# Performance work log

Hardware: AMD Instinct MI355X
Metric: run time of the kernel (lower is better)

Reference implementation:

```python
import jax, jax.numpy as jnp
import numpy as np

N_QUBITS = 5
N_LAYERS = 2
N_CLASSES = 2
B = 262144
C64 = jnp.complex64

# ---- gate matrices (PennyLane conventions, half-angle) ----

def _ry(t):
    c, s = jnp.cos(t / 2), jnp.sin(t / 2)
    return jnp.stack([jnp.stack([c, -s]), jnp.stack([s, c])]).astype(C64)

def _rz(t):
    e = jnp.exp(-0.5j * t.astype(C64))
    z = jnp.zeros((), C64)
    return jnp.stack([jnp.stack([e, z]), jnp.stack([z, jnp.conj(e)])])

def _rx(t):
    c = jnp.cos(t / 2).astype(C64)
    s = (-1j) * jnp.sin(t / 2).astype(C64)
    return jnp.stack([jnp.stack([c, s]), jnp.stack([s, c])])

def _cry(t):  # control = first wire, target = second
    return jnp.eye(4, dtype=C64).at[2:, 2:].set(_ry(t))

def _crx(t):
    return jnp.eye(4, dtype=C64).at[2:, 2:].set(_rx(t))

CNOT = jnp.array([[1, 0, 0, 0], [0, 1, 0, 0], [0, 0, 0, 1], [0, 0, 1, 0]], C64)
CZ = jnp.array(np.diag([1, 1, 1, -1]), C64)
RX_P = _rx(jnp.float32(np.pi / 2))
RX_M = _rx(jnp.float32(-np.pi / 2))

# ---- statevector application; state shape [B,2,2,2,2,2] ----

def apply_1q(state, gate, w):
    s = jnp.moveaxis(state, w + 1, -1)
    sh = s.shape
    s = s.reshape(-1, 2) @ gate.T
    return jnp.moveaxis(s.reshape(sh), -1, w + 1)

def apply_2q(state, gate, w0, w1):
    s = jnp.moveaxis(state, (w0 + 1, w1 + 1), (-2, -1))
    sh = s.shape
    s = s.reshape(-1, 4) @ gate.T
    return jnp.moveaxis(s.reshape(sh), (-2, -1), (w0 + 1, w1 + 1))

def conv_block(state, w, wires):
    n = len(wires)
    for i in range(n):
        a, b = wires[i], wires[(i + 1) % n]
        state = apply_2q(state, CNOT, a, b)
        state = apply_1q(state, _rz(w[i]), b)
        state = apply_2q(state, CNOT, a, b)
        state = apply_1q(state, RX_P, a)
        state = apply_1q(state, RX_P, b)
        state = apply_2q(state, CNOT, a, b)
        state = apply_1q(state, RX_M, a)
        state = apply_1q(state, RX_M, b)
        state = apply_2q(state, CZ, a, b)
        state = apply_1q(state, _rz(w[i + 2]), b)
        state = apply_2q(state, CZ, a, b)
    return state

def pool_block(state, w, wires):
    a, b = wires[0], wires[1]
    state = apply_1q(state, _ry(w[0]), a)
    state = apply_1q(state, _ry(w[1]), b)
    state = apply_2q(state, CNOT, a, b)
    state = apply_2q(state, _cry(w[0]), b, a)  # CRY control=b target=a
    state = apply_2q(state, _crx(w[1]), a, b)  # CRX control=a target=b
    state = apply_2q(state, CNOT, b, a)
    return state

def _circuit(x, conv, pool):
    # AngleEmbedding(rotation='Y') from |0..0>: per-qubit amp [cos(x/2), sin(x/2)]
    amps = jnp.stack([jnp.cos(x / 2), jnp.sin(x / 2)], axis=-1).astype(C64)  # [B,5,2]
    a = [amps[:, q] for q in range(N_QUBITS)]
    state = jnp.einsum('bi,bj,bk,bl,bm->bijklm', *a)  # [B,2,2,2,2,2]
    wires = list(range(N_QUBITS))
    for l in range(N_LAYERS):
        state = conv_block(state, conv[l], wires)
        state = pool_block(state, pool[l], wires)
        wires = wires[1:]
    p = jnp.abs(state) ** 2
    evs = []
    for w in wires[:N_CLASSES]:
        axes = tuple(q + 1 for q in range(N_QUBITS) if q != w)
        pw = p.sum(axis=axes)  # [B,2]
        evs.append(pw[:, 0] - pw[:, 1])
    return jnp.stack(evs, axis=-1)  # [B,2]


def setup_inputs() -> dict:
    key = jax.random.key(0)
    ks = jax.random.split(key, 5)
    x = jax.random.normal(ks[0], (B, N_QUBITS), jnp.float32)
    conv = jax.random.normal(ks[1], (N_LAYERS, 3 * N_QUBITS), jnp.float32)
    pool = jax.random.normal(ks[2], (N_LAYERS, 2), jnp.float32)
    fc_w = jax.random.normal(ks[3], (N_CLASSES, N_CLASSES), jnp.float32) * 0.5
    fc_b = jax.random.normal(ks[4], (N_CLASSES,), jnp.float32) * 0.1
    return {"x": x, "conv": conv, "pool": pool, "fc_w": fc_w, "fc_b": fc_b}


def reference(x, conv, pool, fc_w, fc_b):
    z = _circuit(x, conv, pool)  # [B,2] PauliZ expvals
    return z @ fc_w.T + fc_b
```

## Files before the change

kernel.cpp:

```cpp
#include <hip/hip_runtime.h>
#include <math.h>

#define NQ 5
#define DIM 32


__device__ inline void rx_step(float& ax, float& ay, int m, float c, float sn) {
    float px = __shfl_xor(ax, m);
    float py = __shfl_xor(ay, m);
    float nx = c * ax + sn * py;
    float ny = c * ay - sn * px;
    ax = nx; ay = ny;
}

__device__ inline void ry_step(float& ax, float& ay, int k, int m, float c, float sn) {
    float px = __shfl_xor(ax, m);
    float py = __shfl_xor(ay, m);
    float f = (k & m) ? sn : -sn;
    ax = c * ax + f * px;
    ay = c * ay + f * py;
}

__device__ inline void cnot_step(float& ax, float& ay, int k, int mc, int mt) {
    float px = __shfl_xor(ax, mt);
    float py = __shfl_xor(ay, mt);
    if (k & mc) { ax = px; ay = py; }
}

__global__ __launch_bounds__(1024) void build_A_kernel(
        const float* __restrict__ conv, const float* __restrict__ pool,
        const float* __restrict__ fcw, float* __restrict__ A) {
    const int tid  = threadIdx.x;
    const int col  = tid >> 5;
    const int k    = tid & 31;

    float ax = (k == col) ? 1.0f : 0.0f;
    float ay = 0.0f;

    int wires[NQ] = {0, 1, 2, 3, 4};
    int nw = NQ;
    const float S2 = 0.70710678118654752440f;

    #pragma unroll
    for (int l = 0; l < 2; ++l) {
        const float* w = conv + l * 15;
        for (int i = 0; i < nw; ++i) {
            const int a = wires[i], b = wires[(i + 1) % nw];
            const int ma = 16 >> a, mb = 16 >> b;
            {
                float c, sn; __sincosf(0.5f * w[i], &sn, &c);
                float eim = ((((k & ma) != 0) ^ (((k & mb) != 0)))) ? sn : -sn;
                float nx = c * ax - eim * ay;
                float ny = c * ay + eim * ax;
                ax = nx; ay = ny;
            }
            rx_step(ax, ay, ma, S2, S2);
            rx_step(ax, ay, mb, S2, S2);
            cnot_step(ax, ay, k, ma, mb);
            rx_step(ax, ay, ma, S2, -S2);
            rx_step(ax, ay, mb, S2, -S2);
            {
                float c, sn; __sincosf(0.5f * w[i + 2], &sn, &c);
                float eim = (k & mb) ? sn : -sn;
                float nx = c * ax - eim * ay;
                float ny = c * ay + eim * ax;
                ax = nx; ay = ny;
            }
        }
        {
            const float* pw = pool + l * 2;
            const int a = wires[0], b = wires[1];
            const int ma = 16 >> a, mb = 16 >> b;
            float c0, s0v, c1, s1v;
            __sincosf(0.5f * pw[0], &s0v, &c0);
            __sincosf(0.5f * pw[1], &s1v, &c1);
            ry_step(ax, ay, k, ma, c0, s0v);
            ry_step(ax, ay, k, mb, c1, s1v);
            cnot_step(ax, ay, k, ma, mb);
            {
                float px = __shfl_xor(ax, ma);
                float py = __shfl_xor(ay, ma);
                if (k & mb) {
                    float f = (k & ma) ? s0v : -s0v;
                    float nx = c0 * ax + f * px;
                    float ny = c0 * ay + f * py;
                    ax = nx; ay = ny;
                }
            }
            {
                float px = __shfl_xor(ax, mb);
                float py = __shfl_xor(ay, mb);
                if (k & ma) {
                    float nx = c1 * ax + s1v * py;
                    float ny = c1 * ay - s1v * px;
                    ax = nx; ay = ny;
                }
            }
            cnot_step(ax, ay, k, mb, ma);
        }
        for (int q = 0; q < nw - 1; ++q) wires[q] = wires[q + 1];
        nw--;
    }

    __shared__ float2 U[DIM][DIM + 1];
    U[col][k] = make_float2(ax, ay);
    __syncthreads();

    const int s = tid >> 5, t = tid & 31;
    const float w00 = fcw[0], w01 = fcw[1], w10 = fcw[2], w11 = fcw[3];
    float acc0 = 0.0f, acc1 = 0.0f;
    #pragma unroll
    for (int kk = 0; kk < DIM; ++kk) {
        float2 us = U[s][kk];
        float2 ut = U[t][kk];
        float d = us.x * ut.x + us.y * ut.y;
        float d2 = (kk & 4) ? -d : d;
        float d3 = (kk & 2) ? -d : d;
        acc0 += w00 * d2 + w01 * d3;
        acc1 += w10 * d2 + w11 * d3;
    }
    float f0 = (t < s) ? 0.0f : ((t == s) ? acc0 : 2.0f * acc0);
    float f1 = (t < s) ? 0.0f : ((t == s) ? acc1 : 2.0f * acc1);
    A[s * DIM + t]             = f0;
    A[DIM * DIM + s * DIM + t] = f1;
}

__global__ __launch_bounds__(256) void qcnn_eval_kernel(
        const float* __restrict__ x, const float* __restrict__ A,
        const float* __restrict__ fcb, float* __restrict__ out, int nB) {
    __shared__ float xs[256 * NQ];
    const int base = blockIdx.x * 256 * NQ;
    #pragma unroll
    for (int i = 0; i < NQ; ++i) {
        int idx = threadIdx.x + i * 256;
        xs[idx] = x[base + idx];
    }
    __syncthreads();

    const int b = blockIdx.x * 256 + threadIdx.x;
    if (b >= nB) return;

    float cs[NQ], sn[NQ];
    #pragma unroll
    for (int q = 0; q < NQ; ++q) {
        float xv = xs[threadIdx.x * NQ + q];
        __sincosf(0.5f * xv, &sn[q], &cs[q]);
    }
    float v01[4];
    v01[0] = cs[0] * cs[1]; v01[1] = cs[0] * sn[1];
    v01[2] = sn[0] * cs[1]; v01[3] = sn[0] * sn[1];
    float v23[4];
    v23[0] = cs[2] * cs[3]; v23[1] = cs[2] * sn[3];
    v23[2] = sn[2] * cs[3]; v23[3] = sn[2] * sn[3];
    float v234[8];
    #pragma unroll
    for (int i = 0; i < 4; ++i) {
        v234[2 * i]     = v23[i] * cs[4];
        v234[2 * i + 1] = v23[i] * sn[4];
    }
    float s0[DIM];
    #pragma unroll
    for (int s = 0; s < DIM; ++s) s0[s] = v01[s >> 3] * v234[s & 7];

    float res0 = fcb[0], res1 = fcb[1];
    #pragma unroll
    for (int si = 0; si < DIM; ++si) {
        float row0 = 0.0f, row1 = 0.0f;
        #pragma unroll
        for (int t = si; t < DIM; ++t) {
            row0 = fmaf(A[si * DIM + t],             s0[t], row0);
            row1 = fmaf(A[DIM * DIM + si * DIM + t], s0[t], row1);
        }
        res0 = fmaf(s0[si], row0, res0);
        res1 = fmaf(s0[si], row1, res1);
    }
    reinterpret_cast<float2*>(out)[b] = make_float2(res0, res1);
}

extern "C" void kernel_launch(void* const* d_in, const int* in_sizes, int n_in,
                              void* d_out, int out_size, void* d_ws, size_t ws_size,
                              hipStream_t stream) {
    const float* x    = (const float*)d_in[0];
    const float* conv = (const float*)d_in[1];
    const float* pool = (const float*)d_in[2];
    const float* fcw  = (const float*)d_in[3];
    const float* fcb  = (const float*)d_in[4];
    float* out = (float*)d_out;
    float* A   = (float*)d_ws;

    const int nB = in_sizes[0] / NQ;

    hipLaunchKernelGGL(build_A_kernel, dim3(1), dim3(1024), 0, stream,
                       conv, pool, fcw, A);
    hipLaunchKernelGGL(qcnn_eval_kernel, dim3((nB + 255) / 256), dim3(256), 0, stream,
                       x, A, fcb, out, nB);
}
```

Before: 83.79 us.

## Expand quadratic form into Pauli basis and evaluate via nested trig polynomial

The precomputed 32x32 quadratic-form matrix is projected onto the Pauli basis of 243 coefficients per class, each qubit contributing I, Z or X. This works because the input state is a product of RY rotations, so each term becomes a product of 1, cos x or sin x per qubit. The eval kernel now evaluates a nested Horner-like tensor contraction (27+9+3+1 levels) per class, in place of the ~528-term quadratic form. This cuts FMAs and coefficient loads per sample but adds a projection step to the single-block setup kernel.

```diff
diff --git a/kernel.cpp b/kernel.cpp
--- a/kernel.cpp
+++ b/kernel.cpp
@@ -27,9 +27,10 @@
     if (k & mc) { ax = px; ay = py; }
 }
 
-__global__ __launch_bounds__(1024) void build_A_kernel(
+__global__ __launch_bounds__(1024) void build_coef_kernel(
         const float* __restrict__ conv, const float* __restrict__ pool,
-        const float* __restrict__ fcw, float* __restrict__ A) {
+        const float* __restrict__ fcw, const float* __restrict__ fcb,
+        float* __restrict__ coef) {
     const int tid  = threadIdx.x;
     const int col  = tid >> 5;
     const int k    = tid & 31;
@@ -119,15 +120,44 @@
         acc0 += w00 * d2 + w01 * d3;
         acc1 += w10 * d2 + w11 * d3;
     }
-    float f0 = (t < s) ? 0.0f : ((t == s) ? acc0 : 2.0f * acc0);
-    float f1 = (t < s) ? 0.0f : ((t == s) ? acc1 : 2.0f * acc1);
-    A[s * DIM + t]             = f0;
-    A[DIM * DIM + s * DIM + t] = f1;
+    __shared__ float A0[DIM][DIM + 1], A1[DIM][DIM + 1];
+    A0[s][t] = acc0;
+    A1[s][t] = acc1;
+    __syncthreads();
+
+    if (tid < 486) {
+        const int cls = tid / 243;
+        int r = tid % 243;
+        const int pp = r;
+        int dgt[NQ];
+        dgt[4] = r % 3; r /= 3;
+        dgt[3] = r % 3; r /= 3;
+        dgt[2] = r % 3; r /= 3;
+        dgt[1] = r % 3; r /= 3;
+        dgt[0] = r;
+        int xmask = 0, zmask = 0;
+        #pragma unroll
+        for (int q = 0; q < NQ; ++q) {
+            const int m = 16 >> q;
+            if (dgt[q] == 1) zmask |= m;
+            else if (dgt[q] == 2) xmask |= m;
+        }
+        const float (*Ac)[DIM + 1] = cls ? A1 : A0;
+        float val = 0.0f;
+        #pragma unroll
+        for (int ss = 0; ss < DIM; ++ss) {
+            float a = Ac[ss][ss ^ xmask];
+            val += (__popc(ss & zmask) & 1) ? -a : a;
+        }
+        val *= (1.0f / 32.0f);
+        if (pp == 0) val += fcb[cls];
+        coef[cls * 243 + pp] = val;
+    }
 }
 
 __global__ __launch_bounds__(256) void qcnn_eval_kernel(
-        const float* __restrict__ x, const float* __restrict__ A,
-        const float* __restrict__ fcb, float* __restrict__ out, int nB) {
+        const float* __restrict__ x, const float* __restrict__ C,
+        float* __restrict__ out, int nB) {
     __shared__ float xs[256 * NQ];
     const int base = blockIdx.x * 256 * NQ;
     #pragma unroll
@@ -140,41 +170,36 @@
     const int b = blockIdx.x * 256 + threadIdx.x;
     if (b >= nB) return;
 
-    float cs[NQ], sn[NQ];
+    float u[NQ], v[NQ];
     #pragma unroll
     for (int q = 0; q < NQ; ++q) {
         float xv = xs[threadIdx.x * NQ + q];
-        __sincosf(0.5f * xv, &sn[q], &cs[q]);
-    }
-    float v01[4];
-    v01[0] = cs[0] * cs[1]; v01[1] = cs[0] * sn[1];
-    v01[2] = sn[0] * cs[1]; v01[3] = sn[0] * sn[1];
-    float v23[4];
-    v23[0] = cs[2] * cs[3]; v23[1] = cs[2] * sn[3];
-    v23[2] = sn[2] * cs[3]; v23[3] = sn[2] * sn[3];
-    float v234[8];
-    #pragma unroll
-    for (int i = 0; i < 4; ++i) {
-        v234[2 * i]     = v23[i] * cs[4];
-        v234[2 * i + 1] = v23[i] * sn[4];
-    }
-    float s0[DIM];
-    #pragma unroll
-    for (int s = 0; s < DIM; ++s) s0[s] = v01[s >> 3] * v234[s & 7];
-
-    float res0 = fcb[0], res1 = fcb[1];
-    #pragma unroll
-    for (int si = 0; si < DIM; ++si) {
-        float row0 = 0.0f, row1 = 0.0f;
-        #pragma unroll
-        for (int t = si; t < DIM; ++t) {
-            row0 = fmaf(A[si * DIM + t],             s0[t], row0);
-            row1 = fmaf(A[DIM * DIM + si * DIM + t], s0[t], row1);
-        }
-        res0 = fmaf(s0[si], row0, res0);
-        res1 = fmaf(s0[si], row1, res1);
-    }
-    reinterpret_cast<float2*>(out)[b] = make_float2(res0, res1);
+        __sincosf(xv, &v[q], &u[q]);
+    }
+
+    float res[2];
+    #pragma unroll
+    for (int cls = 0; cls < 2; ++cls) {
+        const float* Cc = C + cls * 243;
+        float lvl3[27];
+        #pragma unroll
+        for (int i = 0; i < 27; ++i) {
+            float e0 = fmaf(v[4], Cc[9 * i + 2], fmaf(u[4], Cc[9 * i + 1], Cc[9 * i + 0]));
+            float e1 = fmaf(v[4], Cc[9 * i + 5], fmaf(u[4], Cc[9 * i + 4], Cc[9 * i + 3]));
+            float e2 = fmaf(v[4], Cc[9 * i + 8], fmaf(u[4], Cc[9 * i + 7], Cc[9 * i + 6]));
+            lvl3[i] = fmaf(v[3], e2, fmaf(u[3], e1, e0));
+        }
+        float lvl2[9];
+        #pragma unroll
+        for (int i = 0; i < 9; ++i)
+            lvl2[i] = fmaf(v[2], lvl3[3 * i + 2], fmaf(u[2], lvl3[3 * i + 1], lvl3[3 * i]));
+        float lvl1[3];
+        #pragma unroll
+        for (int i = 0; i < 3; ++i)
+            lvl1[i] = fmaf(v[1], lvl2[3 * i + 2], fmaf(u[1], lvl2[3 * i + 1], lvl2[3 * i]));
+        res[cls] = fmaf(v[0], lvl1[2], fmaf(u[0], lvl1[1], lvl1[0]));
+    }
+    reinterpret_cast<float2*>(out)[b] = make_float2(res[0], res[1]);
 }
 
 extern "C" void kernel_launch(void* const* d_in, const int* in_sizes, int n_in,
@@ -185,13 +210,13 @@
     const float* pool = (const float*)d_in[2];
     const float* fcw  = (const float*)d_in[3];
     const float* fcb  = (const float*)d_in[4];
-    float* out = (float*)d_out;
-    float* A   = (float*)d_ws;
+    float* out  = (float*)d_out;
+    float* coef = (float*)d_ws;
 
     const int nB = in_sizes[0] / NQ;
 
-    hipLaunchKernelGGL(build_A_kernel, dim3(1), dim3(1024), 0, stream,
-                       conv, pool, fcw, A);
+    hipLaunchKernelGGL(build_coef_kernel, dim3(1), dim3(1024), 0, stream,
+                       conv, pool, fcw, fcb, coef);
     hipLaunchKernelGGL(qcnn_eval_kernel, dim3((nB + 255) / 256), dim3(256), 0, stream,
-                       x, A, fcb, out, nB);
-}
+                       x, coef, out, nB);
+}
```

New measurement: 83.16 us. Within noise of the previous version (-0.8%).
